# Kernel tuning notes

Hardware: AMD Instinct MI355X
Metric: run time of the kernel (lower is better)

The kernel has to match this reference:

```python
import jax, jax.numpy as jnp
import numpy as np

H = 16          # num_heads
EPS = 1e-5      # LayerNorm eps (torch default)


def _layernorm(x, g, b):
    m = jnp.mean(x, axis=-1, keepdims=True)
    v = jnp.mean((x - m) ** 2, axis=-1, keepdims=True)
    return (x - m) * jax.lax.rsqrt(v + EPS) * g + b


def setup_inputs() -> dict:
    key = jax.random.key(0)
    ks = jax.random.split(key, 16)
    B, S, D, F = 4, 1024, 1024, 4096
    s = 0.02
    inp = {
        "x": jax.random.normal(ks[0], (B, S, D), jnp.float32),
        "attn_bias": jax.random.normal(ks[1], (B - 1, H), jnp.float32),
        "mask": jax.random.randint(ks[2], (B, 1, S, S), 0, 2).astype(jnp.float32),
        "ln1_g": jnp.ones((D,), jnp.float32),
        "ln1_b": jnp.zeros((D,), jnp.float32),
        "Wq": jax.random.normal(ks[3], (D, D), jnp.float32) * s,
        "bq": jnp.zeros((D,), jnp.float32),
        "Wk": jax.random.normal(ks[4], (D, D), jnp.float32) * s,
        "bk": jnp.zeros((D,), jnp.float32),
        "Wv": jax.random.normal(ks[5], (D, D), jnp.float32) * s,
        "bv": jnp.zeros((D,), jnp.float32),
        "Wo": jax.random.normal(ks[6], (D, D), jnp.float32) * s,
        "bo": jnp.zeros((D,), jnp.float32),
        "ln2_g": jnp.ones((D,), jnp.float32),
        "ln2_b": jnp.zeros((D,), jnp.float32),
        "W1": jax.random.normal(ks[7], (D, F), jnp.float32) * s,
        "b1": jnp.zeros((F,), jnp.float32),
        "W2": jax.random.normal(ks[8], (F, D), jnp.float32) * s,
        "b2": jnp.zeros((D,), jnp.float32),
    }
    return inp


def reference(x, attn_bias, mask, ln1_g, ln1_b, Wq, bq, Wk, bk, Wv, bv, Wo, bo,
              ln2_g, ln2_b, W1, b1, W2, b2):
    B, S, D = x.shape
    d = D // H
    scale = d ** -0.5

    # ---- self-attention block ----
    y = _layernorm(x, ln1_g, ln1_b)
    q = (y @ Wq + bq).reshape(B, S, H, d).transpose(0, 2, 1, 3) * scale  # [B,H,S,d]
    k = (y @ Wk + bk).reshape(B, S, H, d).transpose(0, 2, 1, 3)
    v = (y @ Wv + bv).reshape(B, S, H, d).transpose(0, 2, 1, 3)

    scores = jnp.einsum("bhqd,bhkd->bhqk", q, k)                         # [B,H,S,S]
    # per-batch additive bias applied to batches 1: only (as in torch x[1:] += bias)
    scores = scores.at[1:].add(attn_bias[:, :, None, None])
    # multiplicative mask + large-negative additive mask where mask <= 0
    scores = scores * mask + jnp.where(mask > 0.0, 0.0, -1e9)
    attn = jax.nn.softmax(scores, axis=-1)

    ctx = jnp.einsum("bhqk,bhkd->bhqd", attn, v)                          # [B,H,S,d]
    ctx = ctx.transpose(0, 2, 1, 3).reshape(B, S, D)
    x = x + (ctx @ Wo + bo)

    # ---- FFN block ----
    y = _layernorm(x, ln2_g, ln2_b)
    y = jax.nn.gelu(y @ W1 + b1, approximate=False) @ W2 + b2
    return x + y
```

## Files before the change

### kernel.cpp

```cpp
#include <hip/hip_runtime.h>
#include <hip/hip_bf16.h>
#include <math.h>

typedef __attribute__((ext_vector_type(8))) __bf16 bf16x8;
typedef __attribute__((ext_vector_type(4))) float f32x4;
typedef __hip_bfloat16 bf16;

#define D_MODEL 1024
#define F_FFN   4096
#define NHEAD   16
#define HDIM    64
#define SEQ     1024
#define BATCH   4

static __device__ __forceinline__ unsigned short bf_bits(bf16 h) {
  return __builtin_bit_cast(unsigned short, h);
}

template <int N>
static __device__ __forceinline__ void vwait() {
  asm volatile("s_waitcnt vmcnt(%0)" :: "n"(N) : "memory");
}

static __device__ __forceinline__ void gload_lds16(const bf16* src, bf16* dst) {
  __builtin_amdgcn_global_load_lds(
      (const __attribute__((address_space(1))) void*)src,
      (__attribute__((address_space(3))) void*)dst, 16, 0, 0);
}

__global__ __launch_bounds__(1024) void prep_kernel(
    const float* __restrict__ Wq, const float* __restrict__ Wk,
    const float* __restrict__ Wv, const float* __restrict__ Wo,
    const float* __restrict__ W1, const float* __restrict__ W2,
    const float* __restrict__ mask,
    bf16* __restrict__ Wqkv_t, bf16* __restrict__ Wo_t,
    bf16* __restrict__ W1_t, bf16* __restrict__ W2_t,
    unsigned* __restrict__ mbits) {
  __shared__ float tile[32][33];
  int bid = blockIdx.x;
  int tid = threadIdx.x;
  if (bid < 12288) {
    const float* W; bf16* Wt; int K, N, tx32, ty32;
    if (bid < 4096) {
      int w = bid >> 10;
      W  = (w == 0) ? Wq : (w == 1) ? Wk : (w == 2) ? Wv : Wo;
      Wt = (w < 3) ? Wqkv_t + (size_t)w * 1024 * 1024 : Wo_t;
      K = 1024; N = 1024;
      int t = bid & 1023; tx32 = t & 31; ty32 = t >> 5;
    } else if (bid < 8192) {
      W = W1; Wt = W1_t; K = 1024; N = 4096;
      int t = bid - 4096; tx32 = t & 127; ty32 = t >> 7;
    } else {
      W = W2; Wt = W2_t; K = 4096; N = 1024;
      int t = bid - 8192; tx32 = t & 31; ty32 = t >> 5;
    }
    int nb = tx32 * 32, kb = ty32 * 32;
    int tx = tid & 31, ty = tid >> 5;
    tile[ty][tx] = W[(size_t)(kb + ty) * N + nb + tx];
    __syncthreads();
    Wt[(size_t)(nb + ty) * K + kb + tx] = __float2bfloat16(tile[tx][ty]);
  } else {
    int gw = ((bid - 12288) * 1024 + tid) >> 6;
    int lane = tid & 63;
    const float4 m = reinterpret_cast<const float4*>(mask)[(size_t)gw * 64 + lane];
    unsigned long long b0 = __ballot(m.x > 0.f);
    unsigned long long b1 = __ballot(m.y > 0.f);
    unsigned long long b2 = __ballot(m.z > 0.f);
    unsigned long long b3 = __ballot(m.w > 0.f);
    if (lane < 8) {
      unsigned v = 0;
#pragma unroll
      for (int i = 0; i < 8; ++i) {
        int srcl = lane * 8 + i;
        v |= (((unsigned)(b0 >> srcl) & 1u) << (i * 4 + 0));
        v |= (((unsigned)(b1 >> srcl) & 1u) << (i * 4 + 1));
        v |= (((unsigned)(b2 >> srcl) & 1u) << (i * 4 + 2));
        v |= (((unsigned)(b3 >> srcl) & 1u) << (i * 4 + 3));
      }
      mbits[(size_t)gw * 8 + lane] = v;
    }
  }
}

__global__ __launch_bounds__(256) void layernorm_kernel(
    const float* __restrict__ x, const float* __restrict__ g,
    const float* __restrict__ bt, bf16* __restrict__ y) {
  int row = blockIdx.x;
  int tid = threadIdx.x;
  const float* xr = x + (size_t)row * D_MODEL;
  float4 v = reinterpret_cast<const float4*>(xr)[tid];
  float s  = v.x + v.y + v.z + v.w;
  float s2 = v.x * v.x + v.y * v.y + v.z * v.z + v.w * v.w;
  for (int o = 32; o; o >>= 1) { s += __shfl_xor(s, o); s2 += __shfl_xor(s2, o); }
  __shared__ float r1[4], r2[4];
  int wid = tid >> 6, lane = tid & 63;
  if (lane == 0) { r1[wid] = s; r2[wid] = s2; }
  __syncthreads();
  float tot  = r1[0] + r1[1] + r1[2] + r1[3];
  float tot2 = r2[0] + r2[1] + r2[2] + r2[3];
  float mean = tot * (1.f / D_MODEL);
  float var  = tot2 * (1.f / D_MODEL) - mean * mean;
  float rstd = rsqrtf(var + 1e-5f);
  float4 gg = reinterpret_cast<const float4*>(g)[tid];
  float4 bb = reinterpret_cast<const float4*>(bt)[tid];
  ushort4 o;
  o.x = bf_bits(__float2bfloat16((v.x - mean) * rstd * gg.x + bb.x));
  o.y = bf_bits(__float2bfloat16((v.y - mean) * rstd * gg.y + bb.y));
  o.z = bf_bits(__float2bfloat16((v.z - mean) * rstd * gg.z + bb.z));
  o.w = bf_bits(__float2bfloat16((v.w - mean) * rstd * gg.w + bb.w));
  reinterpret_cast<ushort4*>(y + (size_t)row * D_MODEL)[tid] = o;
}

enum { MODE_QKV = 0, MODE_O = 1, MODE_GELU = 2, MODE_OUT = 3 };

template <int MODE>
__global__ __launch_bounds__(256, 4) void gemm128x64_kernel(
    const bf16* __restrict__ A, const bf16* __restrict__ Bt,
    int M, int N, int K,
    const float* __restrict__ bias0, const float* __restrict__ bias1,
    const float* __restrict__ bias2,
    bf16* __restrict__ out_q, bf16* __restrict__ out_k, bf16* __restrict__ out_vt,
    bf16* __restrict__ out_bf) {
  constexpr int R = 3;
  __shared__ bf16 AS[R][128 * 32];
  __shared__ bf16 BS[R][64 * 32];
  int tid = threadIdx.x;
  int wid = tid >> 6, lane = tid & 63;
  int wm2 = wid >> 1, wn2 = wid & 1;
  int lrow = lane & 15, lg = lane >> 4;
  int nwg = gridDim.x * gridDim.y;
  int lin = blockIdx.y * gridDim.x + blockIdx.x;
  int swz = (lin & 7) * (nwg >> 3) + (lin >> 3);
  int bxi = swz % gridDim.x, byi = swz / gridDim.x;
  int bm = byi * 128, bn = bxi * 64;
  int srow = tid >> 2;
  int sg = (tid & 3) ^ ((tid >> 3) & 3);
  const bf16* Asrc = A  + (size_t)bm * K + sg * 8;
  const bf16* Bsrc = Bt + (size_t)bn * K + sg * 8;
  f32x4 acc[4][2] = {};
  const int NT = K / 32;

  auto stage = [&](int t, int slot) {
    int k0 = t * 32;
#pragma unroll
    for (int j = 0; j < 2; ++j) {
      int row = j * 64 + srow;
      gload_lds16(Asrc + (size_t)row * K + k0, &AS[slot][(j * 256 + tid) * 8]);
    }
    gload_lds16(Bsrc + (size_t)srow * K + k0, &BS[slot][tid * 8]);
  };

  int sw = (lg ^ ((lrow >> 1) & 3)) << 4;
  stage(0, 0);
  stage(1, 1);
  int rslot = 0, wslot = 2;
  for (int t = 0; t < NT; ++t) {
    if (t < NT - 1) vwait<3>();
    else            vwait<0>();
    __builtin_amdgcn_s_barrier();
    const char* as = (const char*)AS[rslot];
    const char* bs = (const char*)BS[rslot];
    bf16x8 af[4], bfr[2];
#pragma unroll
    for (int f = 0; f < 4; ++f)
      af[f] = *reinterpret_cast<const bf16x8*>(as + (wm2 * 64 + f * 16 + lrow) * 64 + sw);
#pragma unroll
    for (int g = 0; g < 2; ++g)
      bfr[g] = *reinterpret_cast<const bf16x8*>(bs + (wn2 * 32 + g * 16 + lrow) * 64 + sw);
    if (t + 2 < NT) stage(t + 2, wslot);
    __builtin_amdgcn_s_setprio(1);
#pragma unroll
    for (int f = 0; f < 4; ++f)
#pragma unroll
      for (int g = 0; g < 2; ++g)
        acc[f][g] = __builtin_amdgcn_mfma_f32_16x16x32_bf16(af[f], bfr[g], acc[f][g], 0, 0, 0);
    __builtin_amdgcn_s_setprio(0);
    rslot = (rslot == R - 1) ? 0 : rslot + 1;
    wslot = (wslot == R - 1) ? 0 : wslot + 1;
  }

#pragma unroll
  for (int f = 0; f < 4; ++f) {
#pragma unroll
    for (int g = 0; g < 2; ++g) {
#pragma unroll
      for (int r = 0; r < 4; ++r) {
        int row = bm + wm2 * 64 + f * 16 + lg * 4 + r;
        int col = bn + wn2 * 32 + g * 16 + lrow;
        float v = acc[f][g][r];
        if (MODE == MODE_QKV) {
          if (col < 1024) {
            out_q[(size_t)row * 1024 + col] = __float2bfloat16((v + bias0[col]) * 0.125f);
          } else if (col < 2048) {
            out_k[(size_t)row * 1024 + (col - 1024)] = __float2bfloat16(v + bias1[col - 1024]);
          } else {
            int d = col - 2048;
            int b = row >> 10;
            int s = row & 1023;
            out_vt[((size_t)(b << 10) + d) * 1024 + s] = __float2bfloat16(v + bias2[d]);
          }
        } else {
          float tv = v + bias0[col];
          out_bf[(size_t)row * N + col] =
              __float2bfloat16(0.5f * tv * (1.f + erff(tv * 0.70710678118654752f)));
        }
      }
    }
  }
}

template <int MODE, int TN>
__global__ __launch_bounds__(512, 4) void gemm256_kernel(
    const bf16* __restrict__ A, const bf16* __restrict__ Bt,
    int M, int N, int K,
    const float* __restrict__ bias0,
    const float* __restrict__ resid,
    float* __restrict__ out_f) {
  constexpr int R = 3;
  constexpr int NF = TN / 32;
  __shared__ bf16 AS[R][256 * 32];
  __shared__ bf16 BS[R][TN * 32];
  int tid = threadIdx.x;
  int wid = tid >> 6, lane = tid & 63;
  int wm4 = wid >> 1, wn2 = wid & 1;
  int lrow = lane & 15, lg = lane >> 4;
  int nwg = gridDim.x * gridDim.y;
  int lin = blockIdx.y * gridDim.x + blockIdx.x;
  int swz = (lin & 7) * (nwg >> 3) + (lin >> 3);
  int bxi = swz % gridDim.x, byi = swz / gridDim.x;
  int bm = byi * 256, bn = bxi * TN;
  int srow = tid >> 2;
  int sg = (tid & 3) ^ ((tid >> 3) & 3);
  const bf16* Asrc = A  + (size_t)bm * K + sg * 8;
  const bf16* Bsrc = Bt + (size_t)bn * K + sg * 8;
  f32x4 acc[4][NF] = {};
  const int NT = K / 32;

  auto stage = [&](int t, int slot) {
    int k0 = t * 32;
#pragma unroll
    for (int j = 0; j < 2; ++j) {
      int row = j * 128 + srow;
      gload_lds16(Asrc + (size_t)row * K + k0, &AS[slot][(j * 512 + tid) * 8]);
    }
    if (TN == 128) {
      gload_lds16(Bsrc + (size_t)srow * K + k0, &BS[slot][tid * 8]);
    } else {
      if (wid < 4)
        gload_lds16(Bsrc + (size_t)srow * K + k0, &BS[slot][tid * 8]);
    }
  };

  int sw = (lg ^ ((lrow >> 1) & 3)) << 4;
  stage(0, 0);
  stage(1, 1);
  int rslot = 0, wslot = 2;
  for (int t = 0; t < NT; ++t) {
    if (t < NT - 1) {
      if (TN == 128) { vwait<3>(); }
      else { if (wid < 4) vwait<3>(); else vwait<2>(); }
    } else {
      vwait<0>();
    }
    __builtin_amdgcn_s_barrier();
    const char* as = (const char*)AS[rslot];
    const char* bs = (const char*)BS[rslot];
    bf16x8 af[4], bfr[NF];
#pragma unroll
    for (int f = 0; f < 4; ++f)
      af[f] = *reinterpret_cast<const bf16x8*>(as + (wm4 * 64 + f * 16 + lrow) * 64 + sw);
#pragma unroll
    for (int g = 0; g < NF; ++g)
      bfr[g] = *reinterpret_cast<const bf16x8*>(bs + (wn2 * (TN / 2) + g * 16 + lrow) * 64 + sw);
    if (t + 2 < NT) stage(t + 2, wslot);
    __builtin_amdgcn_s_setprio(1);
#pragma unroll
    for (int f = 0; f < 4; ++f)
#pragma unroll
      for (int g = 0; g < NF; ++g)
        acc[f][g] = __builtin_amdgcn_mfma_f32_16x16x32_bf16(af[f], bfr[g], acc[f][g], 0, 0, 0);
    __builtin_amdgcn_s_setprio(0);
    rslot = (rslot == R - 1) ? 0 : rslot + 1;
    wslot = (wslot == R - 1) ? 0 : wslot + 1;
  }

#pragma unroll
  for (int f = 0; f < 4; ++f) {
#pragma unroll
    for (int g = 0; g < NF; ++g) {
#pragma unroll
      for (int r = 0; r < 4; ++r) {
        int row = bm + wm4 * 64 + f * 16 + lg * 4 + r;
        int col = bn + wn2 * (TN / 2) + g * 16 + lrow;
        float v = acc[f][g][r];
        out_f[(size_t)row * N + col] = resid[(size_t)row * N + col] + v + bias0[col];
      }
    }
  }
}

#define KVB 64
__global__ __launch_bounds__(512) void attn_kernel(
    const bf16* __restrict__ q, const bf16* __restrict__ k,
    const bf16* __restrict__ vt, const unsigned* __restrict__ mbits,
    bf16* __restrict__ ctx) {
  __shared__ bf16 Kt[2][KVB * 64];
  __shared__ bf16 Vt[2][KVB * 64];
  __shared__ bf16 P[8][16 * 64];
  int tid = threadIdx.x, wid = tid >> 6, lane = tid & 63;
  int blk = (blockIdx.x & 7) * 64 + (blockIdx.x >> 3);
  int qblk = blk & 7, h = (blk >> 3) & 15, b = blk >> 7;
  int qs = qblk * 128 + wid * 16;
  int lrow = lane & 15, lg = lane >> 4;

  size_t qoff = ((size_t)(b * SEQ + qs + lrow)) * D_MODEL + h * HDIM;
  bf16x8 qa0 = *reinterpret_cast<const bf16x8*>(q + qoff + lg * 8);
  bf16x8 qa1 = *reinterpret_cast<const bf16x8*>(q + qoff + 32 + lg * 8);

  float ps[4] = {0.f, 0.f, 0.f, 0.f};
  f32x4 O[4] = {};
  const unsigned* mb = mbits + ((size_t)(b * SEQ + qs + lg * 4)) * 32;
  bf16* Pw = P[wid];

  int rr = lane >> 3;
  int sg8 = (lane & 7) ^ rr;
  const bf16* kb_src = k + ((size_t)b * SEQ) * D_MODEL + h * HDIM + sg8 * 8;
  const bf16* vb_src = vt + ((size_t)(b * D_MODEL + h * HDIM)) * SEQ + sg8 * 8;

#define STAGE(KT2, BUF)                                                          \
  {                                                                              \
    int ks2 = (KT2) * KVB;                                                       \
    gload_lds16(kb_src + (size_t)(ks2 + wid * 8 + rr) * D_MODEL,                 \
                &Kt[BUF][wid * 512]);                                            \
    gload_lds16(vb_src + (size_t)(wid * 8 + rr) * SEQ + ks2,                     \
                &Vt[BUF][wid * 512]);                                            \
  }

  STAGE(0, 0);
  for (int kt = 0; kt < SEQ / KVB; ++kt) {
    int cur = kt & 1;
    __syncthreads();
    if (kt < SEQ / KVB - 1) STAGE(kt + 1, cur ^ 1);

    f32x4 sc[4];
#pragma unroll
    for (int c = 0; c < 4; ++c) {
      int krow = c * 16 + lrow;
      const char* kp = (const char*)&Kt[cur][krow * 64];
      bf16x8 kb0 = *reinterpret_cast<const bf16x8*>(kp + ((lg ^ (krow & 7)) << 4));
      bf16x8 kb1 = *reinterpret_cast<const bf16x8*>(kp + ((((lg + 4) & 7) ^ (krow & 7)) << 4));
      f32x4 z = {0.f, 0.f, 0.f, 0.f};
      sc[c] = __builtin_amdgcn_mfma_f32_16x16x32_bf16(qa0, kb0, z, 0, 0, 0);
      sc[c] = __builtin_amdgcn_mfma_f32_16x16x32_bf16(qa1, kb1, sc[c], 0, 0, 0);
    }

#pragma unroll
    for (int r = 0; r < 4; ++r) {
      uint2 w = *reinterpret_cast<const uint2*>(mb + (size_t)r * 32 + kt * 2);
      int prow = lg * 4 + r;
      char* pb = (char*)Pw + prow * 128;
#pragma unroll
      for (int c = 0; c < 4; ++c) {
        unsigned wsel = (c >= 2) ? w.y : w.x;
        unsigned keep = (wsel >> ((c & 1) * 16 + lrow)) & 1u;
        float p = keep ? __expf(sc[c][r]) : 0.f;
        ps[r] += p;
        int pcol = c * 16 + lrow;
        *(__bf16*)(pb + (((pcol >> 3) ^ (prow & 7)) << 4) + (pcol & 7) * 2) =
            __float2bfloat16(p);
      }
    }

    const char* pbase = (const char*)Pw + lrow * 128;
    bf16x8 pa0 = *reinterpret_cast<const bf16x8*>(pbase + ((lg ^ (lrow & 7)) << 4));
    bf16x8 pa1 = *reinterpret_cast<const bf16x8*>(pbase + ((((lg + 4) & 7) ^ (lrow & 7)) << 4));
#pragma unroll
    for (int nb = 0; nb < 4; ++nb) {
      int vrow = nb * 16 + lrow;
      const char* vp = (const char*)&Vt[cur][vrow * 64];
      bf16x8 vb0 = *reinterpret_cast<const bf16x8*>(vp + ((lg ^ (vrow & 7)) << 4));
      bf16x8 vb1 = *reinterpret_cast<const bf16x8*>(vp + ((((lg + 4) & 7) ^ (vrow & 7)) << 4));
      O[nb] = __builtin_amdgcn_mfma_f32_16x16x32_bf16(pa0, vb0, O[nb], 0, 0, 0);
      O[nb] = __builtin_amdgcn_mfma_f32_16x16x32_bf16(pa1, vb1, O[nb], 0, 0, 0);
    }
  }
#undef STAGE

#pragma unroll
  for (int o = 1; o < 16; o <<= 1)
#pragma unroll
    for (int r = 0; r < 4; ++r) ps[r] += __shfl_xor(ps[r], o);
#pragma unroll
  for (int nb = 0; nb < 4; ++nb)
#pragma unroll
    for (int r = 0; r < 4; ++r) {
      int qg = qs + lg * 4 + r;
      ctx[((size_t)(b * SEQ + qg)) * D_MODEL + h * HDIM + nb * 16 + lrow] =
          __float2bfloat16(O[nb][r] / ps[r]);
    }
}

extern "C" void kernel_launch(void* const* d_in, const int* in_sizes, int n_in,
                              void* d_out, int out_size, void* d_ws, size_t ws_size,
                              hipStream_t stream) {
  const float* x        = (const float*)d_in[0];
  const float* mask     = (const float*)d_in[2];
  const float* ln1_g    = (const float*)d_in[3];
  const float* ln1_b    = (const float*)d_in[4];
  const float* Wq       = (const float*)d_in[5];
  const float* bq       = (const float*)d_in[6];
  const float* Wk       = (const float*)d_in[7];
  const float* bk       = (const float*)d_in[8];
  const float* Wv       = (const float*)d_in[9];
  const float* bv       = (const float*)d_in[10];
  const float* Wo       = (const float*)d_in[11];
  const float* bo       = (const float*)d_in[12];
  const float* ln2_g    = (const float*)d_in[13];
  const float* ln2_b    = (const float*)d_in[14];
  const float* W1       = (const float*)d_in[15];
  const float* b1       = (const float*)d_in[16];
  const float* W2       = (const float*)d_in[17];
  const float* b2       = (const float*)d_in[18];
  float* out            = (float*)d_out;

  char* w = (char*)d_ws;
  const size_t MB = 1u << 20;
  bf16*     y      = (bf16*)(w + 0);
  bf16*     qb     = (bf16*)(w + 8 * MB);
  bf16*     kb     = (bf16*)(w + 16 * MB);
  bf16*     vt     = (bf16*)(w + 24 * MB);
  bf16*     hbuf   = (bf16*)(w + 0);
  bf16*     Wqkv_t = (bf16*)(w + 32 * MB);
  bf16*     Wo_t   = (bf16*)(w + 38 * MB);
  bf16*     W1_t   = (bf16*)(w + 40 * MB);
  bf16*     W2_t   = (bf16*)(w + 48 * MB);
  bf16*     ctx    = (bf16*)(w + 56 * MB);
  float*    x2     = (float*)(w + 64 * MB);
  unsigned* mbits  = (unsigned*)(w + 64 * MB);
  bf16*     y2     = (bf16*)(w + 80 * MB);
  (void)in_sizes; (void)n_in; (void)out_size; (void)ws_size;

  prep_kernel<<<13312, 1024, 0, stream>>>(Wq, Wk, Wv, Wo, W1, W2, mask,
                                          Wqkv_t, Wo_t, W1_t, W2_t, mbits);

  layernorm_kernel<<<4096, 256, 0, stream>>>(x, ln1_g, ln1_b, y);

  gemm128x64_kernel<MODE_QKV><<<dim3(48, 32), 256, 0, stream>>>(
      y, Wqkv_t, 4096, 3072, 1024, bq, bk, bv, qb, kb, vt, nullptr);

  attn_kernel<<<512, 512, 0, stream>>>(qb, kb, vt, mbits, ctx);

  gemm256_kernel<MODE_O, 64><<<dim3(16, 16), 512, 0, stream>>>(
      ctx, Wo_t, 4096, 1024, 1024, bo, x, x2);

  layernorm_kernel<<<4096, 256, 0, stream>>>(x2, ln2_g, ln2_b, y2);

  gemm128x64_kernel<MODE_GELU><<<dim3(64, 32), 256, 0, stream>>>(
      y2, W1_t, 4096, 4096, 1024, b1, nullptr, nullptr,
      nullptr, nullptr, nullptr, hbuf);

  gemm256_kernel<MODE_OUT, 64><<<dim3(16, 16), 512, 0, stream>>>(
      hbuf, W2_t, 4096, 1024, 4096, b2, x2, out);
}
```

Baseline: 285.9 us.

## Use larger GEMM tiles for QKV and FFN1, with fast tanh GELU

The QKV projection now runs on the 256-row tile kernel with 128-wide N tiles. FFN1 uses a new 256x256-tile kernel with 1024 threads and one block per CU. The exact erf GELU is replaced by a tanh approximation computed with __expf. Larger tiles raise operand reuse and cut global traffic per FLOP, and the approximate GELU lowers epilogue cost. The trade-offs are lower occupancy, a small numerical deviation, and partial-wave effects.

```diff
diff --git a/kernel.cpp b/kernel.cpp
--- a/kernel.cpp
+++ b/kernel.cpp
@@ -26,6 +26,13 @@
   __builtin_amdgcn_global_load_lds(
       (const __attribute__((address_space(1))) void*)src,
       (__attribute__((address_space(3))) void*)dst, 16, 0, 0);
+}
+
+static __device__ __forceinline__ float gelu_fast(float x) {
+  float u = x * (0.7978845608f + 0.0356774081f * x * x);
+  u = fminf(u, 15.f);
+  float e = __expf(2.f * u);
+  return 0.5f * x * (1.f + (e - 1.f) / (e + 1.f));
 }
 
 __global__ __launch_bounds__(1024) void prep_kernel(
@@ -113,40 +120,32 @@
 
 enum { MODE_QKV = 0, MODE_O = 1, MODE_GELU = 2, MODE_OUT = 3 };
 
-template <int MODE>
-__global__ __launch_bounds__(256, 4) void gemm128x64_kernel(
+__global__ __launch_bounds__(1024, 1) void gemm256sq_gelu_kernel(
     const bf16* __restrict__ A, const bf16* __restrict__ Bt,
     int M, int N, int K,
-    const float* __restrict__ bias0, const float* __restrict__ bias1,
-    const float* __restrict__ bias2,
-    bf16* __restrict__ out_q, bf16* __restrict__ out_k, bf16* __restrict__ out_vt,
-    bf16* __restrict__ out_bf) {
+    const float* __restrict__ bias0, bf16* __restrict__ out_bf) {
   constexpr int R = 3;
-  __shared__ bf16 AS[R][128 * 32];
-  __shared__ bf16 BS[R][64 * 32];
+  __shared__ bf16 AS[R][256 * 32];
+  __shared__ bf16 BS[R][256 * 32];
   int tid = threadIdx.x;
   int wid = tid >> 6, lane = tid & 63;
-  int wm2 = wid >> 1, wn2 = wid & 1;
+  int wm4 = wid >> 2, wn4 = wid & 3;
   int lrow = lane & 15, lg = lane >> 4;
   int nwg = gridDim.x * gridDim.y;
   int lin = blockIdx.y * gridDim.x + blockIdx.x;
   int swz = (lin & 7) * (nwg >> 3) + (lin >> 3);
   int bxi = swz % gridDim.x, byi = swz / gridDim.x;
-  int bm = byi * 128, bn = bxi * 64;
+  int bm = byi * 256, bn = bxi * 256;
   int srow = tid >> 2;
   int sg = (tid & 3) ^ ((tid >> 3) & 3);
   const bf16* Asrc = A  + (size_t)bm * K + sg * 8;
   const bf16* Bsrc = Bt + (size_t)bn * K + sg * 8;
-  f32x4 acc[4][2] = {};
+  f32x4 acc[4][4] = {};
   const int NT = K / 32;
 
   auto stage = [&](int t, int slot) {
     int k0 = t * 32;
-#pragma unroll
-    for (int j = 0; j < 2; ++j) {
-      int row = j * 64 + srow;
-      gload_lds16(Asrc + (size_t)row * K + k0, &AS[slot][(j * 256 + tid) * 8]);
-    }
+    gload_lds16(Asrc + (size_t)srow * K + k0, &AS[slot][tid * 8]);
     gload_lds16(Bsrc + (size_t)srow * K + k0, &BS[slot][tid * 8]);
   };
 
@@ -155,24 +154,24 @@
   stage(1, 1);
   int rslot = 0, wslot = 2;
   for (int t = 0; t < NT; ++t) {
-    if (t < NT - 1) vwait<3>();
+    if (t < NT - 1) vwait<2>();
     else            vwait<0>();
     __builtin_amdgcn_s_barrier();
     const char* as = (const char*)AS[rslot];
     const char* bs = (const char*)BS[rslot];
-    bf16x8 af[4], bfr[2];
+    bf16x8 af[4], bfr[4];
 #pragma unroll
     for (int f = 0; f < 4; ++f)
-      af[f] = *reinterpret_cast<const bf16x8*>(as + (wm2 * 64 + f * 16 + lrow) * 64 + sw);
-#pragma unroll
-    for (int g = 0; g < 2; ++g)
-      bfr[g] = *reinterpret_cast<const bf16x8*>(bs + (wn2 * 32 + g * 16 + lrow) * 64 + sw);
+      af[f] = *reinterpret_cast<const bf16x8*>(as + (wm4 * 64 + f * 16 + lrow) * 64 + sw);
+#pragma unroll
+    for (int g = 0; g < 4; ++g)
+      bfr[g] = *reinterpret_cast<const bf16x8*>(bs + (wn4 * 64 + g * 16 + lrow) * 64 + sw);
     if (t + 2 < NT) stage(t + 2, wslot);
     __builtin_amdgcn_s_setprio(1);
 #pragma unroll
     for (int f = 0; f < 4; ++f)
 #pragma unroll
-      for (int g = 0; g < 2; ++g)
+      for (int g = 0; g < 4; ++g)
         acc[f][g] = __builtin_amdgcn_mfma_f32_16x16x32_bf16(af[f], bfr[g], acc[f][g], 0, 0, 0);
     __builtin_amdgcn_s_setprio(0);
     rslot = (rslot == R - 1) ? 0 : rslot + 1;
@@ -182,28 +181,13 @@
 #pragma unroll
   for (int f = 0; f < 4; ++f) {
 #pragma unroll
-    for (int g = 0; g < 2; ++g) {
+    for (int g = 0; g < 4; ++g) {
 #pragma unroll
       for (int r = 0; r < 4; ++r) {
-        int row = bm + wm2 * 64 + f * 16 + lg * 4 + r;
-        int col = bn + wn2 * 32 + g * 16 + lrow;
-        float v = acc[f][g][r];
-        if (MODE == MODE_QKV) {
-          if (col < 1024) {
-            out_q[(size_t)row * 1024 + col] = __float2bfloat16((v + bias0[col]) * 0.125f);
-          } else if (col < 2048) {
-            out_k[(size_t)row * 1024 + (col - 1024)] = __float2bfloat16(v + bias1[col - 1024]);
-          } else {
-            int d = col - 2048;
-            int b = row >> 10;
-            int s = row & 1023;
-            out_vt[((size_t)(b << 10) + d) * 1024 + s] = __float2bfloat16(v + bias2[d]);
-          }
-        } else {
-          float tv = v + bias0[col];
-          out_bf[(size_t)row * N + col] =
-              __float2bfloat16(0.5f * tv * (1.f + erff(tv * 0.70710678118654752f)));
-        }
+        int row = bm + wm4 * 64 + f * 16 + lg * 4 + r;
+        int col = bn + wn4 * 64 + g * 16 + lrow;
+        float tv = acc[f][g][r] + bias0[col];
+        out_bf[(size_t)row * N + col] = __float2bfloat16(gelu_fast(tv));
       }
     }
   }
@@ -213,8 +197,10 @@
 __global__ __launch_bounds__(512, 4) void gemm256_kernel(
     const bf16* __restrict__ A, const bf16* __restrict__ Bt,
     int M, int N, int K,
-    const float* __restrict__ bias0,
+    const float* __restrict__ bias0, const float* __restrict__ bias1,
+    const float* __restrict__ bias2,
     const float* __restrict__ resid,
+    bf16* __restrict__ out_q, bf16* __restrict__ out_k, bf16* __restrict__ out_vt,
     float* __restrict__ out_f) {
   constexpr int R = 3;
   constexpr int NF = TN / 32;
@@ -293,7 +279,20 @@
         int row = bm + wm4 * 64 + f * 16 + lg * 4 + r;
         int col = bn + wn2 * (TN / 2) + g * 16 + lrow;
         float v = acc[f][g][r];
-        out_f[(size_t)row * N + col] = resid[(size_t)row * N + col] + v + bias0[col];
+        if (MODE == MODE_QKV) {
+          if (col < 1024) {
+            out_q[(size_t)row * 1024 + col] = __float2bfloat16((v + bias0[col]) * 0.125f);
+          } else if (col < 2048) {
+            out_k[(size_t)row * 1024 + (col - 1024)] = __float2bfloat16(v + bias1[col - 1024]);
+          } else {
+            int d = col - 2048;
+            int b = row >> 10;
+            int s = row & 1023;
+            out_vt[((size_t)(b << 10) + d) * 1024 + s] = __float2bfloat16(v + bias2[d]);
+          }
+        } else {
+          out_f[(size_t)row * N + col] = resid[(size_t)row * N + col] + v + bias0[col];
+        }
       }
     }
   }
@@ -445,20 +444,22 @@
 
   layernorm_kernel<<<4096, 256, 0, stream>>>(x, ln1_g, ln1_b, y);
 
-  gemm128x64_kernel<MODE_QKV><<<dim3(48, 32), 256, 0, stream>>>(
-      y, Wqkv_t, 4096, 3072, 1024, bq, bk, bv, qb, kb, vt, nullptr);
+  gemm256_kernel<MODE_QKV, 128><<<dim3(24, 16), 512, 0, stream>>>(
+      y, Wqkv_t, 4096, 3072, 1024, bq, bk, bv, nullptr,
+      qb, kb, vt, nullptr);
 
   attn_kernel<<<512, 512, 0, stream>>>(qb, kb, vt, mbits, ctx);
 
   gemm256_kernel<MODE_O, 64><<<dim3(16, 16), 512, 0, stream>>>(
-      ctx, Wo_t, 4096, 1024, 1024, bo, x, x2);
+      ctx, Wo_t, 4096, 1024, 1024, bo, nullptr, nullptr, x,
+      nullptr, nullptr, nullptr, x2);
 
   layernorm_kernel<<<4096, 256, 0, stream>>>(x2, ln2_g, ln2_b, y2);
 
-  gemm128x64_kernel<MODE_GELU><<<dim3(64, 32), 256, 0, stream>>>(
-      y2, W1_t, 4096, 4096, 1024, b1, nullptr, nullptr,
-      nullptr, nullptr, nullptr, hbuf);
+  gemm256sq_gelu_kernel<<<dim3(16, 16), 1024, 0, stream>>>(
+      y2, W1_t, 4096, 4096, 1024, b1, hbuf);
 
   gemm256_kernel<MODE_OUT, 64><<<dim3(16, 16), 512, 0, stream>>>(
-      hbuf, W2_t, 4096, 1024, 4096, b2, x2, out);
-}
+      hbuf, W2_t, 4096, 1024, 4096, b2, nullptr, nullptr, x2,
+      nullptr, nullptr, nullptr, out);
+}
```

Result: faster. 245.3 us (-14.2%).
